# Optimization experiments

Measured on AMD Instinct MI355X. Metric: run time of the kernel, lower is better.

Reference implementation:

```python
import jax, jax.numpy as jnp
import numpy as np
from jax import lax

EPS = 1e-5


def _conv3x3(x, w):
    # NCHW input, OIHW weight, stride 1, padding 1
    return lax.conv_general_dilated(
        x, w, window_strides=(1, 1), padding=((1, 1), (1, 1)),
        dimension_numbers=("NCHW", "OIHW", "NCHW"))


def _batchnorm(y, gamma, beta):
    # training-mode BN: batch statistics over N,H,W
    mean = jnp.mean(y, axis=(0, 2, 3), keepdims=True)
    var = jnp.var(y, axis=(0, 2, 3), keepdims=True)
    inv = lax.rsqrt(var + EPS)
    return (y - mean) * inv * gamma[None, :, None, None] + beta[None, :, None, None]


def setup_inputs() -> dict:
    key = jax.random.key(0)
    k1, k2, k3 = jax.random.split(key, 3)
    N, C, H, W = 32, 128, 56, 56
    x = jax.random.normal(k1, (N, C, H, W), dtype=jnp.float32)
    w1 = jax.random.normal(k2, (C, C, 3, 3), dtype=jnp.float32) * 0.05
    w2 = jax.random.normal(k3, (C, C, 3, 3), dtype=jnp.float32) * 0.05
    gamma1 = jnp.ones((C,), jnp.float32)
    beta1 = jnp.zeros((C,), jnp.float32)
    gamma2 = jnp.ones((C,), jnp.float32)
    beta2 = jnp.zeros((C,), jnp.float32)
    return {"x": x, "w1": w1, "gamma1": gamma1, "beta1": beta1,
            "w2": w2, "gamma2": gamma2, "beta2": beta2}


def reference(x, w1, gamma1, beta1, w2, gamma2, beta2):
    # binarized conv weights: sign(w), with straight-through estimator
    # (matches torch's .data swap, which routes grads to the original weight)
    w1b = w1 + lax.stop_gradient(jnp.sign(w1) - w1)
    w2b = w2 + lax.stop_gradient(jnp.sign(w2) - w2)
    out = jax.nn.relu(_batchnorm(_conv3x3(x, w1b), gamma1, beta1))
    out = _batchnorm(_conv3x3(out, w2b), gamma2, beta2)
    out = out + x  # identity shortcut (stride=1, in_planes==planes)
    return jax.nn.relu(out)
```

## Files before the change

kernel.cpp:

```cpp
#include <hip/hip_runtime.h>

typedef unsigned short u16;
typedef unsigned short u16x8 __attribute__((ext_vector_type(8)));
typedef __bf16 bf16x8 __attribute__((ext_vector_type(8)));
typedef float f32x4 __attribute__((ext_vector_type(4)));

#define HW 3136
#define NPIX 100352
#define PADR 3364
#define KD 1152

__device__ __forceinline__ float bf2f(u16 u) {
    unsigned int x = ((unsigned int)u) << 16;
    return __builtin_bit_cast(float, x);
}
__device__ __forceinline__ u16 f2bf(float f) {
    unsigned int u = __builtin_bit_cast(unsigned int, f);
    return (u16)((u + 0x7FFFu + ((u >> 16) & 1u)) >> 16);
}
__device__ __forceinline__ void gload16(const void* g, void* l) {
    __builtin_amdgcn_global_load_lds(
        (const __attribute__((address_space(1))) unsigned int*)g,
        (__attribute__((address_space(3))) unsigned int*)l, 16, 0, 0);
}

__global__ void setup_kernel(const float* __restrict__ w1, const float* __restrict__ w2,
                             u16* __restrict__ Bm1, u16* __restrict__ Bm2,
                             u16* __restrict__ xbp) {
    const int b = blockIdx.x;
    const int t = threadIdx.x;
    if (b < 1152) {
        const float* w = (b < 576) ? w1 : w2;
        u16* Bm = (b < 576) ? Bm1 : Bm2;
        int i = (b % 576) * 256 + t;
        int k  = i / KD;
        int kk = i - k * KD;
        int c  = kk & 127;
        int rs = kk >> 7;
        float v = w[(size_t)(k * 128 + c) * 9 + rs];
        float sv = (v > 0.f) ? 1.f : ((v < 0.f) ? -1.f : 0.f);
        Bm[i] = f2bf(sv);
    } else {
        int idx = (b - 1152) * 256 + t;
        int pix = idx >> 4;
        int cc  = idx & 15;
        int n  = pix / 228;
        int pb = pix - n * 228;
        int h, w;
        if (pb < 58)       { h = 0;  w = pb; }
        else if (pb < 116) { h = 57; w = pb - 58; }
        else { int q = pb - 116; h = 1 + (q >> 1); w = (q & 1) ? 57 : 0; }
        u16x8 z = {};
        *(u16x8*)(xbp + ((size_t)(n * PADR + h * 58 + w)) * 128 + cc * 8) = z;
    }
}

__global__ void x_to_nhwc(const float* __restrict__ x, u16* __restrict__ xbp) {
    __shared__ float tile[32][65];
    const int t = threadIdx.x;
    const int n = blockIdx.y;
    const int ct = blockIdx.x & 3;
    const int pt = blockIdx.x >> 2;
    const int c0 = ct * 32, p0 = pt * 64;
    {
        const int c  = t >> 3;
        const int pw = (t & 7) * 8;
        const size_t ib = ((size_t)(n * 128 + c0 + c)) * HW + p0 + pw;
        const float4 v0 = *(const float4*)(x + ib);
        const float4 v1 = *(const float4*)(x + ib + 4);
        tile[c][pw + 0] = v0.x; tile[c][pw + 1] = v0.y;
        tile[c][pw + 2] = v0.z; tile[c][pw + 3] = v0.w;
        tile[c][pw + 4] = v1.x; tile[c][pw + 5] = v1.y;
        tile[c][pw + 6] = v1.z; tile[c][pw + 7] = v1.w;
    }
    __syncthreads();
    {
        const int pl = t >> 2;
        const int cs = (t & 3) * 8;
        const int p  = p0 + pl;
        const int h  = p / 56;
        const int w  = p - h * 56;
        u16x8 o;
#pragma unroll
        for (int j = 0; j < 8; ++j) o[j] = f2bf(tile[cs + j][pl]);
        *(u16x8*)(xbp + ((size_t)(n * PADR + (h + 1) * 58 + (w + 1))) * 128 + c0 + cs) = o;
    }
}

#define A0 0
#define B0 8192
#define A1 16384
#define B1 24576

__global__ __launch_bounds__(256, 2) void conv_mfma(
    const u16* __restrict__ xbp, const u16* __restrict__ Bm,
    u16* __restrict__ y, float2* __restrict__ partial)
{
    __shared__ __align__(16) u16 smem[32768];
    const int t = threadIdx.x;
    const int bid = blockIdx.x;
    const int pm0 = bid * 128;
    const int wid  = t >> 6;
    const int lane = t & 63;
    const int lrow = lane & 15;
    const int lhk  = lane >> 4;
    const int m0 = (wid >> 1) * 64;
    const int n0 = (wid & 1) * 64;

    const int rsub = lane >> 3;
    const int csrc = (lane & 7) ^ rsub;
    int apix[4], bbase[4];
#pragma unroll
    for (int j = 0; j < 4; ++j) {
        int row = (wid * 4 + j) * 8 + rsub;
        int ps  = pm0 + row;
        int n   = ps / HW;
        int rem = ps - n * HW;
        int h   = rem / 56;
        int w   = rem - h * 56;
        apix[j]  = (n * PADR + (h + 1) * 58 + (w + 1)) * 128 + csrc * 8;
        bbase[j] = row * KD + csrc * 8;
    }

    f32x4 acc[4][4] = {};

#define STAGE(AOFF, BOFF, p) do {                                              \
    int rs_ = (p) >> 1; int r_ = rs_ / 3; int s_ = rs_ - r_ * 3;               \
    int ash = ((r_ - 1) * 58 + (s_ - 1)) * 128 + ((p) & 1) * 64;               \
    int bsh = (p) * 64;                                                        \
    _Pragma("unroll")                                                          \
    for (int j = 0; j < 4; ++j) {                                              \
        gload16(xbp + apix[j] + ash, smem + (AOFF) + (wid * 4 + j) * 512);     \
        gload16(Bm + bbase[j] + bsh, smem + (BOFF) + (wid * 4 + j) * 512);     \
    } } while (0)

#define COMPUTE(AOFF, BOFF) do {                                               \
    _Pragma("unroll")                                                          \
    for (int kc = 0; kc < 2; ++kc) {                                           \
        bf16x8 af[4], bv[4];                                                   \
        _Pragma("unroll")                                                      \
        for (int mi = 0; mi < 4; ++mi) {                                       \
            int ck = (((kc << 2) | lhk) ^ (lrow & 7)) << 3;                    \
            af[mi] = *(const bf16x8*)&smem[(AOFF) + (m0 + mi * 16 + lrow) * 64 + ck]; \
        }                                                                      \
        _Pragma("unroll")                                                      \
        for (int ni = 0; ni < 4; ++ni) {                                       \
            int ck = (((kc << 2) | lhk) ^ (lrow & 7)) << 3;                    \
            bv[ni] = *(const bf16x8*)&smem[(BOFF) + (n0 + ni * 16 + lrow) * 64 + ck]; \
        }                                                                      \
        __builtin_amdgcn_s_setprio(1);                                         \
        _Pragma("unroll")                                                      \
        for (int mi = 0; mi < 4; ++mi)                                         \
        _Pragma("unroll")                                                      \
            for (int ni = 0; ni < 4; ++ni)                                     \
                acc[mi][ni] = __builtin_amdgcn_mfma_f32_16x16x32_bf16(         \
                    af[mi], bv[ni], acc[mi][ni], 0, 0, 0);                     \
        __builtin_amdgcn_s_setprio(0);                                         \
    } } while (0)

#define WAITBAR8() asm volatile("s_waitcnt vmcnt(8)\n\ts_barrier" ::: "memory")
#define WAITBAR0() asm volatile("s_waitcnt vmcnt(0)\n\ts_barrier" ::: "memory")
#define BAR()      asm volatile("s_barrier" ::: "memory")

    STAGE(A0, B0, 0);
    STAGE(A1, B1, 1);
#pragma unroll 1
    for (int pp = 0; pp < 16; pp += 2) {
        WAITBAR8();
        COMPUTE(A0, B0);
        BAR();
        STAGE(A0, B0, pp + 2);
        WAITBAR8();
        COMPUTE(A1, B1);
        BAR();
        STAGE(A1, B1, pp + 3);
    }
    WAITBAR8();
    COMPUTE(A0, B0);
    BAR();
    WAITBAR0();
    COMPUTE(A1, B1);
    BAR();
#undef STAGE
#undef COMPUTE
#undef WAITBAR8
#undef WAITBAR0
#undef BAR

    float sv[4], qv[4];
#pragma unroll
    for (int ni = 0; ni < 4; ++ni) {
        float a = 0.f, b = 0.f;
#pragma unroll
        for (int mi = 0; mi < 4; ++mi)
#pragma unroll
            for (int q = 0; q < 4; ++q) { float v = acc[mi][ni][q]; a += v; b += v * v; }
        a += __shfl_xor(a, 16); a += __shfl_xor(a, 32);
        b += __shfl_xor(b, 16); b += __shfl_xor(b, 32);
        sv[ni] = a; qv[ni] = b;
    }
    float2* sred = (float2*)(smem + 20480);
    if (lane < 16) {
#pragma unroll
        for (int ni = 0; ni < 4; ++ni)
            sred[wid * 64 + ni * 16 + lane] = make_float2(sv[ni], qv[ni]);
    }

#pragma unroll
    for (int mi = 0; mi < 4; ++mi)
#pragma unroll
        for (int ni = 0; ni < 4; ++ni)
#pragma unroll
            for (int q = 0; q < 4; ++q)
                smem[(m0 + mi * 16 + lhk * 4 + q) * 136 + n0 + ni * 16 + lrow] =
                    f2bf(acc[mi][ni][q]);
    __syncthreads();
    {
        const int px = t >> 1, half = t & 1;
        const u16* src = &smem[px * 136 + half * 64];
        u16* dst = y + (size_t)(pm0 + px) * 128 + half * 64;
#pragma unroll
        for (int j = 0; j < 8; ++j)
            *(u16x8*)(dst + j * 8) = *(const u16x8*)(src + j * 8);
    }
    if (t < 128) {
        const int ni = (t >> 4) & 3, oc = t & 15, hi = t >> 6;
        float2 u = sred[hi * 64 + ni * 16 + oc];
        float2 v = sred[(hi + 2) * 64 + ni * 16 + oc];
        partial[(size_t)t * 784 + bid] = make_float2(u.x + v.x, u.y + v.y);
    }
}

__global__ void stats_finalize(const float2* __restrict__ partial,
                               const float* __restrict__ gamma, const float* __restrict__ beta,
                               float2* __restrict__ coef) {
    __shared__ float ss[256], ss2[256];
    const int c = blockIdx.x, t = threadIdx.x;
    const float2* pc = partial + (size_t)c * 784;
    float s = 0.f, s2 = 0.f;
    for (int i = t; i < 784; i += 256) { float2 v = pc[i]; s += v.x; s2 += v.y; }
    ss[t] = s; ss2[t] = s2;
    __syncthreads();
    for (int o = 128; o > 0; o >>= 1) {
        if (t < o) { ss[t] += ss[t + o]; ss2[t] += ss2[t + o]; }
        __syncthreads();
    }
    if (t == 0) {
        double mean = (double)ss[0] / (double)NPIX;
        double var  = (double)ss2[0] / (double)NPIX - mean * mean;
        if (var < 0.0) var = 0.0;
        float inv = rsqrtf((float)var + 1e-5f);
        float a = gamma[c] * inv;
        coef[c] = make_float2(a, beta[c] - (float)mean * a);
    }
}

__global__ void bnrelu_kernel(const u16* __restrict__ y, const float2* __restrict__ coef,
                              u16* __restrict__ out1p) {
    __shared__ float2 sc[128];
    const int b = blockIdx.x;
    const int t = threadIdx.x;
    if (b >= 6272) {
        int idx = (b - 6272) * 256 + t;
        int pix = idx >> 4;
        int cc  = idx & 15;
        int n  = pix / 228;
        int pb = pix - n * 228;
        int h, w;
        if (pb < 58)       { h = 0;  w = pb; }
        else if (pb < 116) { h = 57; w = pb - 58; }
        else { int q = pb - 116; h = 1 + (q >> 1); w = (q & 1) ? 57 : 0; }
        u16x8 z = {};
        *(u16x8*)(out1p + ((size_t)(n * PADR + h * 58 + w)) * 128 + cc * 8) = z;
        return;
    }
    if (t < 128) sc[t] = coef[t];
    __syncthreads();
    size_t i = (size_t)b * 256 + t;
    u16x8 v = *(const u16x8*)(y + i * 8);
    int p  = (int)(i >> 4);
    int c0 = (int)(i & 15) * 8;
    int n   = p / HW;
    int rem = p - n * HW;
    int h   = rem / 56;
    int w   = rem - h * 56;
    u16x8 o;
#pragma unroll
    for (int j = 0; j < 8; ++j) {
        float2 k = sc[c0 + j];
        o[j] = f2bf(fmaxf(bf2f(v[j]) * k.x + k.y, 0.f));
    }
    *(u16x8*)(out1p + ((size_t)(n * PADR + (h + 1) * 58 + (w + 1))) * 128 + c0) = o;
}

__global__ void bn_add_relu_nchw(const u16* __restrict__ y2, const float2* __restrict__ coef,
                                 const u16* __restrict__ xbp, float* __restrict__ out) {
    __shared__ float tile[32][65];
    __shared__ float2 sc[32];
    const int t = threadIdx.x;
    const int n = blockIdx.y;
    const int ct = blockIdx.x & 3;
    const int pt = blockIdx.x >> 2;
    const int c0 = ct * 32, p0 = pt * 64;
    if (t < 32) sc[t] = coef[c0 + t];
    __syncthreads();
    {
        const int pl = t >> 2;
        const int cs = (t & 3) * 8;
        const int p  = p0 + pl;
        const int h  = p / 56;
        const int w  = p - h * 56;
        const u16x8 v = *(const u16x8*)(y2 + ((size_t)(n * HW + p)) * 128 + c0 + cs);
        const u16x8 xv = *(const u16x8*)(xbp +
            ((size_t)(n * PADR + (h + 1) * 58 + (w + 1))) * 128 + c0 + cs);
#pragma unroll
        for (int j = 0; j < 8; ++j) {
            float2 k = sc[cs + j];
            tile[cs + j][pl] = bf2f(v[j]) * k.x + k.y + bf2f(xv[j]);
        }
    }
    __syncthreads();
    {
        const int c  = t >> 3;
        const int pw = (t & 7) * 8;
        const size_t ob = ((size_t)(n * 128 + c0 + c)) * HW + p0 + pw;
        float4 o0, o1;
        o0.x = fmaxf(tile[c][pw + 0], 0.f);
        o0.y = fmaxf(tile[c][pw + 1], 0.f);
        o0.z = fmaxf(tile[c][pw + 2], 0.f);
        o0.w = fmaxf(tile[c][pw + 3], 0.f);
        o1.x = fmaxf(tile[c][pw + 4], 0.f);
        o1.y = fmaxf(tile[c][pw + 5], 0.f);
        o1.z = fmaxf(tile[c][pw + 6], 0.f);
        o1.w = fmaxf(tile[c][pw + 7], 0.f);
        *(float4*)(out + ob) = o0;
        *(float4*)(out + ob + 4) = o1;
    }
}

extern "C" void kernel_launch(void* const* d_in, const int* in_sizes, int n_in,
                              void* d_out, int out_size, void* d_ws, size_t ws_size,
                              hipStream_t stream) {
    const float* x  = (const float*)d_in[0];
    const float* w1 = (const float*)d_in[1];
    const float* g1 = (const float*)d_in[2];
    const float* b1 = (const float*)d_in[3];
    const float* w2 = (const float*)d_in[4];
    const float* g2 = (const float*)d_in[5];
    const float* b2 = (const float*)d_in[6];
    float* out = (float*)d_out;
    char* ws = (char*)d_ws;

    u16*    xbp   = (u16*)(ws);
    u16*    ybuf  = (u16*)(ws + 27557888);
    u16*    Bm1   = (u16*)(ws + 53248000);
    u16*    Bm2   = (u16*)(ws + 53542912);
    float2* part  = (float2*)(ws + 53837824);
    float2* cf1   = (float2*)(ws + 54640640);
    float2* cf2   = (float2*)(ws + 54641664);
    u16*    out1p = (u16*)d_out;

    setup_kernel<<<1608, 256, 0, stream>>>(w1, w2, Bm1, Bm2, xbp);
    x_to_nhwc<<<dim3(196, 32), 256, 0, stream>>>(x, xbp);

    conv_mfma<<<784, 256, 0, stream>>>(xbp, Bm1, ybuf, part);
    stats_finalize<<<128, 256, 0, stream>>>(part, g1, b1, cf1);
    bnrelu_kernel<<<6728, 256, 0, stream>>>(ybuf, cf1, out1p);

    conv_mfma<<<784, 256, 0, stream>>>(out1p, Bm2, ybuf, part);
    stats_finalize<<<128, 256, 0, stream>>>(part, g2, b2, cf2);
    bn_add_relu_nchw<<<dim3(196, 32), 256, 0, stream>>>(ybuf, cf2, xbp, out);
}
```

Measured before the change: 150.1 us.

## Replace double-buffered conv pipeline with single-buffer loop and higher occupancy

Removes the two-stage LDS double-buffering with manual vmcnt waits and setprio, and uses a single A/B buffer with __syncthreads around each stage. Shared memory drops from 64KB to 40KB and launch bounds ask for 4 blocks per CU instead of 2, relying on more resident waves to hide global-load latency in place of software prefetch. The risks are that loads are no longer overlapped within a block, and that the higher occupancy target may cap registers and cause spills for the 64-float accumulator.

```diff
diff --git a/kernel.cpp b/kernel.cpp
--- a/kernel.cpp
+++ b/kernel.cpp
@@ -87,16 +87,13 @@
     }
 }
 
-#define A0 0
-#define B0 8192
-#define A1 16384
-#define B1 24576
-
-__global__ __launch_bounds__(256, 2) void conv_mfma(
+__global__ __launch_bounds__(256, 4) void conv_mfma(
     const u16* __restrict__ xbp, const u16* __restrict__ Bm,
     u16* __restrict__ y, float2* __restrict__ partial)
 {
-    __shared__ __align__(16) u16 smem[32768];
+    __shared__ __align__(16) u16 smem[20480];
+    u16* As = smem;
+    u16* Bs = smem + 8192;
     const int t = threadIdx.x;
     const int bid = blockIdx.x;
     const int pm0 = bid * 128;
@@ -124,68 +121,40 @@
 
     f32x4 acc[4][4] = {};
 
-#define STAGE(AOFF, BOFF, p) do {                                              \
-    int rs_ = (p) >> 1; int r_ = rs_ / 3; int s_ = rs_ - r_ * 3;               \
-    int ash = ((r_ - 1) * 58 + (s_ - 1)) * 128 + ((p) & 1) * 64;               \
-    int bsh = (p) * 64;                                                        \
-    _Pragma("unroll")                                                          \
-    for (int j = 0; j < 4; ++j) {                                              \
-        gload16(xbp + apix[j] + ash, smem + (AOFF) + (wid * 4 + j) * 512);     \
-        gload16(Bm + bbase[j] + bsh, smem + (BOFF) + (wid * 4 + j) * 512);     \
-    } } while (0)
-
-#define COMPUTE(AOFF, BOFF) do {                                               \
-    _Pragma("unroll")                                                          \
-    for (int kc = 0; kc < 2; ++kc) {                                           \
-        bf16x8 af[4], bv[4];                                                   \
-        _Pragma("unroll")                                                      \
-        for (int mi = 0; mi < 4; ++mi) {                                       \
-            int ck = (((kc << 2) | lhk) ^ (lrow & 7)) << 3;                    \
-            af[mi] = *(const bf16x8*)&smem[(AOFF) + (m0 + mi * 16 + lrow) * 64 + ck]; \
-        }                                                                      \
-        _Pragma("unroll")                                                      \
-        for (int ni = 0; ni < 4; ++ni) {                                       \
-            int ck = (((kc << 2) | lhk) ^ (lrow & 7)) << 3;                    \
-            bv[ni] = *(const bf16x8*)&smem[(BOFF) + (n0 + ni * 16 + lrow) * 64 + ck]; \
-        }                                                                      \
-        __builtin_amdgcn_s_setprio(1);                                         \
-        _Pragma("unroll")                                                      \
-        for (int mi = 0; mi < 4; ++mi)                                         \
-        _Pragma("unroll")                                                      \
-            for (int ni = 0; ni < 4; ++ni)                                     \
-                acc[mi][ni] = __builtin_amdgcn_mfma_f32_16x16x32_bf16(         \
-                    af[mi], bv[ni], acc[mi][ni], 0, 0, 0);                     \
-        __builtin_amdgcn_s_setprio(0);                                         \
-    } } while (0)
-
-#define WAITBAR8() asm volatile("s_waitcnt vmcnt(8)\n\ts_barrier" ::: "memory")
-#define WAITBAR0() asm volatile("s_waitcnt vmcnt(0)\n\ts_barrier" ::: "memory")
-#define BAR()      asm volatile("s_barrier" ::: "memory")
-
-    STAGE(A0, B0, 0);
-    STAGE(A1, B1, 1);
 #pragma unroll 1
-    for (int pp = 0; pp < 16; pp += 2) {
-        WAITBAR8();
-        COMPUTE(A0, B0);
-        BAR();
-        STAGE(A0, B0, pp + 2);
-        WAITBAR8();
-        COMPUTE(A1, B1);
-        BAR();
-        STAGE(A1, B1, pp + 3);
-    }
-    WAITBAR8();
-    COMPUTE(A0, B0);
-    BAR();
-    WAITBAR0();
-    COMPUTE(A1, B1);
-    BAR();
-#undef STAGE
-#undef COMPUTE
-#undef WAITBAR8
-#undef WAITBAR0
-#undef BAR
+    for (int pp = 0; pp < 18; ++pp) {
+        const int rs_ = pp >> 1;
+        const int r_ = rs_ / 3, s_ = rs_ - r_ * 3;
+        const int ash = ((r_ - 1) * 58 + (s_ - 1)) * 128 + (pp & 1) * 64;
+        const int bsh = pp * 64;
+#pragma unroll
+        for (int j = 0; j < 4; ++j) {
+            gload16(xbp + apix[j] + ash, As + (wid * 4 + j) * 512);
+            gload16(Bm + bbase[j] + bsh, Bs + (wid * 4 + j) * 512);
+        }
+        __syncthreads();
+#pragma unroll
+        for (int kc = 0; kc < 2; ++kc) {
+            bf16x8 af[4], bv[4];
+#pragma unroll
+            for (int mi = 0; mi < 4; ++mi) {
+                int ck = (((kc << 2) | lhk) ^ (lrow & 7)) << 3;
+                af[mi] = *(const bf16x8*)&As[(m0 + mi * 16 + lrow) * 64 + ck];
+            }
+#pragma unroll
+            for (int ni = 0; ni < 4; ++ni) {
+                int ck = (((kc << 2) | lhk) ^ (lrow & 7)) << 3;
+                bv[ni] = *(const bf16x8*)&Bs[(n0 + ni * 16 + lrow) * 64 + ck];
+            }
+#pragma unroll
+            for (int mi = 0; mi < 4; ++mi)
+#pragma unroll
+                for (int ni = 0; ni < 4; ++ni)
+                    acc[mi][ni] = __builtin_amdgcn_mfma_f32_16x16x32_bf16(
+                        af[mi], bv[ni], acc[mi][ni], 0, 0, 0);
+        }
+        __syncthreads();
+    }
 
     float sv[4], qv[4];
 #pragma unroll
@@ -199,7 +168,7 @@
         b += __shfl_xor(b, 16); b += __shfl_xor(b, 32);
         sv[ni] = a; qv[ni] = b;
     }
-    float2* sred = (float2*)(smem + 20480);
+    float2* sred = (float2*)(smem + 17408);
     if (lane < 16) {
 #pragma unroll
         for (int ni = 0; ni < 4; ++ni)
```

Measured after the change: 147.0 us. -2.0%, faster.

## Load conv weight fragments straight to registers and swizzle block order

Applied to the files above, without the earlier changes.

The weight (B) operand no longer goes through LDS. Each wave loads its B MFMA fragments directly from global memory into registers, double-buffered across pipeline stages, so LDS holds only the activation tiles and shrinks. The block index is remapped so that consecutive hardware blocks spread across pixel ranges, which is meant to improve L2 locality. The hand-tuned vmcnt/barrier pipeline is replaced by plain __syncthreads, and the last iteration prefetches one stage past the end. That adds redundant, possibly out-of-range loads and may lose load/compute overlap.

```diff
diff --git a/kernel.cpp b/kernel.cpp
--- a/kernel.cpp
+++ b/kernel.cpp
@@ -87,18 +87,14 @@
     }
 }
 
-#define A0 0
-#define B0 8192
-#define A1 16384
-#define B1 24576
-
-__global__ __launch_bounds__(256, 2) void conv_mfma(
+__global__ __launch_bounds__(256) void conv_mfma(
     const u16* __restrict__ xbp, const u16* __restrict__ Bm,
     u16* __restrict__ y, float2* __restrict__ partial)
 {
-    __shared__ __align__(16) u16 smem[32768];
-    const int t = threadIdx.x;
-    const int bid = blockIdx.x;
+    __shared__ __align__(16) u16 smem[18432];
+    const int t = threadIdx.x;
+    const int bid0 = blockIdx.x;
+    const int bid = (bid0 & 7) * 98 + (bid0 >> 3);
     const int pm0 = bid * 128;
     const int wid  = t >> 6;
     const int lane = t & 63;
@@ -109,7 +105,7 @@
 
     const int rsub = lane >> 3;
     const int csrc = (lane & 7) ^ rsub;
-    int apix[4], bbase[4];
+    int apix[4];
 #pragma unroll
     for (int j = 0; j < 4; ++j) {
         int row = (wid * 4 + j) * 8 + rsub;
@@ -118,74 +114,70 @@
         int rem = ps - n * HW;
         int h   = rem / 56;
         int w   = rem - h * 56;
-        apix[j]  = (n * PADR + (h + 1) * 58 + (w + 1)) * 128 + csrc * 8;
-        bbase[j] = row * KD + csrc * 8;
-    }
+        apix[j] = (n * PADR + (h + 1) * 58 + (w + 1)) * 128 + csrc * 8;
+    }
+    const u16* pB0 = Bm + (n0 +  0 + lrow) * KD + lhk * 8;
+    const u16* pB1 = Bm + (n0 + 16 + lrow) * KD + lhk * 8;
+    const u16* pB2 = Bm + (n0 + 32 + lrow) * KD + lhk * 8;
+    const u16* pB3 = Bm + (n0 + 48 + lrow) * KD + lhk * 8;
 
     f32x4 acc[4][4] = {};
-
-#define STAGE(AOFF, BOFF, p) do {                                              \
+    bf16x8 bA[4][2], bB[4][2];
+
+#define STAGE_A(p, AOFF) do {                                                  \
     int rs_ = (p) >> 1; int r_ = rs_ / 3; int s_ = rs_ - r_ * 3;               \
     int ash = ((r_ - 1) * 58 + (s_ - 1)) * 128 + ((p) & 1) * 64;               \
-    int bsh = (p) * 64;                                                        \
     _Pragma("unroll")                                                          \
-    for (int j = 0; j < 4; ++j) {                                              \
+    for (int j = 0; j < 4; ++j)                                                \
         gload16(xbp + apix[j] + ash, smem + (AOFF) + (wid * 4 + j) * 512);     \
-        gload16(Bm + bbase[j] + bsh, smem + (BOFF) + (wid * 4 + j) * 512);     \
-    } } while (0)
-
-#define COMPUTE(AOFF, BOFF) do {                                               \
+    } while (0)
+
+#define LOADB(dst, p) do {                                                     \
+    dst[0][0] = *(const bf16x8*)(pB0 + (p) * 64);                              \
+    dst[0][1] = *(const bf16x8*)(pB0 + (p) * 64 + 32);                         \
+    dst[1][0] = *(const bf16x8*)(pB1 + (p) * 64);                              \
+    dst[1][1] = *(const bf16x8*)(pB1 + (p) * 64 + 32);                         \
+    dst[2][0] = *(const bf16x8*)(pB2 + (p) * 64);                              \
+    dst[2][1] = *(const bf16x8*)(pB2 + (p) * 64 + 32);                         \
+    dst[3][0] = *(const bf16x8*)(pB3 + (p) * 64);                              \
+    dst[3][1] = *(const bf16x8*)(pB3 + (p) * 64 + 32);                         \
+    } while (0)
+
+#define COMPUTE(AOFF, bset) do {                                               \
     _Pragma("unroll")                                                          \
     for (int kc = 0; kc < 2; ++kc) {                                           \
-        bf16x8 af[4], bv[4];                                                   \
+        bf16x8 af[4];                                                          \
         _Pragma("unroll")                                                      \
         for (int mi = 0; mi < 4; ++mi) {                                       \
             int ck = (((kc << 2) | lhk) ^ (lrow & 7)) << 3;                    \
             af[mi] = *(const bf16x8*)&smem[(AOFF) + (m0 + mi * 16 + lrow) * 64 + ck]; \
         }                                                                      \
         _Pragma("unroll")                                                      \
-        for (int ni = 0; ni < 4; ++ni) {                                       \
-            int ck = (((kc << 2) | lhk) ^ (lrow & 7)) << 3;                    \
-            bv[ni] = *(const bf16x8*)&smem[(BOFF) + (n0 + ni * 16 + lrow) * 64 + ck]; \
-        }                                                                      \
-        __builtin_amdgcn_s_setprio(1);                                         \
-        _Pragma("unroll")                                                      \
         for (int mi = 0; mi < 4; ++mi)                                         \
         _Pragma("unroll")                                                      \
             for (int ni = 0; ni < 4; ++ni)                                     \
                 acc[mi][ni] = __builtin_amdgcn_mfma_f32_16x16x32_bf16(         \
-                    af[mi], bv[ni], acc[mi][ni], 0, 0, 0);                     \
-        __builtin_amdgcn_s_setprio(0);                                         \
+                    af[mi], bset[ni][kc], acc[mi][ni], 0, 0, 0);               \
     } } while (0)
 
-#define WAITBAR8() asm volatile("s_waitcnt vmcnt(8)\n\ts_barrier" ::: "memory")
-#define WAITBAR0() asm volatile("s_waitcnt vmcnt(0)\n\ts_barrier" ::: "memory")
-#define BAR()      asm volatile("s_barrier" ::: "memory")
-
-    STAGE(A0, B0, 0);
-    STAGE(A1, B1, 1);
+    LOADB(bA, 0);
+    STAGE_A(0, 0);
+    __syncthreads();
 #pragma unroll 1
-    for (int pp = 0; pp < 16; pp += 2) {
-        WAITBAR8();
-        COMPUTE(A0, B0);
-        BAR();
-        STAGE(A0, B0, pp + 2);
-        WAITBAR8();
-        COMPUTE(A1, B1);
-        BAR();
-        STAGE(A1, B1, pp + 3);
-    }
-    WAITBAR8();
-    COMPUTE(A0, B0);
-    BAR();
-    WAITBAR0();
-    COMPUTE(A1, B1);
-    BAR();
-#undef STAGE
+    for (int i = 0; i < 9; ++i) {
+        const int pp = 2 * i;
+        STAGE_A(pp + 1, 8192);
+        LOADB(bB, pp + 1);
+        COMPUTE(0, bA);
+        __syncthreads();
+        STAGE_A(pp + 2, 0);
+        LOADB(bA, pp + 2);
+        COMPUTE(8192, bB);
+        __syncthreads();
+    }
+#undef STAGE_A
+#undef LOADB
 #undef COMPUTE
-#undef WAITBAR8
-#undef WAITBAR0
-#undef BAR
 
     float sv[4], qv[4];
 #pragma unroll
@@ -199,7 +191,7 @@
         b += __shfl_xor(b, 16); b += __shfl_xor(b, 32);
         sv[ni] = a; qv[ni] = b;
     }
-    float2* sred = (float2*)(smem + 20480);
+    float2* sred = (float2*)(smem + 17408);
     if (lane < 16) {
 #pragma unroll
         for (int ni = 0; ni < 4; ++ni)
```

Measured after the change: 234.6 us. 56.3% more time.
